# Kernel optimization log

Hardware: AMD Instinct MI355X
Metric: run time of the kernel (lower is better)

Reference implementation:

```python
import jax, jax.numpy as jnp
import numpy as np

D = 6          # atom_dims
K_AA = 17      # atom-atom knn (self dropped -> 16)
K_PE = 16      # point-atom knn
NEG = 0.2      # LeakyReLU slope
EPS = 1e-5     # GroupNorm eps
N_PTS, N_AT = 20000, 8000
H = 2 * D + 1  # MLP hidden width = 13


def lrelu(x):
    return jnp.where(x >= 0, x, NEG * x)


def linear(x, w, b):  # torch Linear convention: w is (out, in)
    return jnp.einsum('...i,oi->...o', x, w) + b


def group_norm(x, gamma, beta, groups):
    n, c = x.shape
    xg = x.reshape(n, groups, c // groups)
    mu = xg.mean(-1, keepdims=True)
    var = ((xg - mu) ** 2).mean(-1, keepdims=True)
    xn = ((xg - mu) * jax.lax.rsqrt(var + EPS)).reshape(n, c)
    return xn * gamma + beta


def knn(x, y, k):
    # squared euclidean distances via gram trick (memory-bound argKmin)
    d2 = jnp.sum(x * x, -1)[:, None] + jnp.sum(y * y, -1)[None, :] - 2.0 * (x @ y.T)
    _, idx = jax.lax.top_k(-jax.lax.stop_gradient(d2), k)
    # recompute dists from gathered coords (matches knn_atoms; differentiable)
    dists = jnp.sum((x[:, None, :] - y[idx]) ** 2, -1)  # (N, k)
    return idx, dists


def mp_block(self_feat, nb_source, idx, dists, w1, b1, w2, b2, gamma, beta, groups):
    n, k = idx.shape
    nb = nb_source[idx]  # (N, k, D) gather
    feat = jnp.concatenate([
        jnp.broadcast_to(self_feat[:, None, :], (n, k, self_feat.shape[1])),
        nb,
        dists[..., None],
    ], axis=-1)  # (N, k, 2D+1)
    msg = linear(lrelu(linear(feat, w1, b1)), w2, b2).sum(1)  # (N, D)
    return self_feat + lrelu(group_norm(msg, gamma, beta, groups))


def setup_inputs() -> dict:
    key = jax.random.key(0)
    ks = jax.random.split(key, 20)
    f = lambda k, s, sc=1.0: jax.random.normal(k, s, jnp.float32) * sc
    inp = {
        'xyz': f(ks[0], (N_PTS, 3), 10.0),
        'atom_xyz': f(ks[1], (N_AT, 3), 10.0),
        'atomtypes': f(ks[2], (N_AT, D)),
        'batch': jnp.zeros((N_PTS,), jnp.int32),
        'atom_batch': jnp.zeros((N_AT,), jnp.int32),
        # transform_types: Linear(D,D) -> LeakyReLU -> Linear(D,D)
        'tt_w1': f(ks[3], (D, D), 0.3), 'tt_b1': f(ks[4], (D,), 0.1),
        'tt_w2': f(ks[5], (D, D), 0.3), 'tt_b2': f(ks[6], (D,), 0.1),
        # atom_atom: 3 layers of Linear(13,13)->LeakyReLU->Linear(13,6), GroupNorm(2,6)
        'aa_w1': f(ks[7], (3, H, H), 0.3), 'aa_b1': f(ks[8], (3, H), 0.1),
        'aa_w2': f(ks[9], (3, D, H), 0.3), 'aa_b2': f(ks[10], (3, D), 0.1),
        'aa_gamma': jnp.ones((3, D), jnp.float32), 'aa_beta': jnp.zeros((3, D), jnp.float32),
        # embed: same shapes
        'em_w1': f(ks[11], (3, H, H), 0.3), 'em_b1': f(ks[12], (3, H), 0.1),
        'em_w2': f(ks[13], (3, D, H), 0.3), 'em_b2': f(ks[14], (3, D), 0.1),
        'em_gamma': jnp.ones((3, D), jnp.float32), 'em_beta': jnp.zeros((3, D), jnp.float32),
    }
    return inp


def reference(xyz, atom_xyz, atomtypes, batch, atom_batch,
              tt_w1, tt_b1, tt_w2, tt_b2,
              aa_w1, aa_b1, aa_w2, aa_b2, aa_gamma, aa_beta,
              em_w1, em_b1, em_w2, em_b2, em_gamma, em_beta):
    # batch / atom_batch are all-zero (single block), so full knn == ranged knn
    at = linear(lrelu(linear(atomtypes, tt_w1, tt_b1)), tt_w2, tt_b2)
    # Atom_Atom_embedding_MP: knn over atoms, drop self (first) neighbor
    idx, dists = knn(atom_xyz, atom_xyz, K_AA)
    idx, dists = idx[:, 1:], dists[:, 1:]
    out = at
    for i in range(3):
        out = mp_block(out, out, idx, dists,
                       aa_w1[i], aa_b1[i], aa_w2[i], aa_b2[i],
                       aa_gamma[i], aa_beta[i], 2)
    # Atom_embedding_MP: points gather from (fixed) atom features
    idx2, dists2 = knn(xyz, atom_xyz, K_PE)
    emb = jnp.ones((xyz.shape[0], D), xyz.dtype)
    for i in range(3):
        emb = mp_block(emb, out, idx2, dists2,
                       em_w1[i], em_b1[i], em_w2[i], em_b2[i],
                       em_gamma[i], em_beta[i], 2)
    return emb
```

## Files before the change

kernel.cpp:

```cpp
#include <hip/hip_runtime.h>
#include <cfloat>
#include <climits>

#define NEG 0.2f
#define GEPS 1e-5f
#define D 6
#define H 13
#define KOUT 16

#define MPAD 8192
#define TILE 1024
#define NTILES 8
#define P1TILES 4
#define QW 8
#define QBLK 32
#define CAP 64
#define KMAX 17
#define MARGIN 0.05f

__device__ __forceinline__ float lrelu(float x){ return x >= 0.f ? x : NEG*x; }

__global__ void prep_kernel(const float* __restrict__ atom_xyz,
                            const float* __restrict__ xyz,
                            const float* __restrict__ at_in,
                            const float* __restrict__ w1, const float* __restrict__ b1,
                            const float* __restrict__ w2, const float* __restrict__ b2,
                            float4* __restrict__ candP, float4* __restrict__ ptsP,
                            float* __restrict__ fa, int n_at, int n_pts){
  int i = blockIdx.x*blockDim.x + threadIdx.x;
  if (i < MPAD){
    if (i < n_at){
      float x = atom_xyz[3*i], y = atom_xyz[3*i+1], z = atom_xyz[3*i+2];
      float sq;
      {
#pragma clang fp contract(off)
        sq = (x*x + y*y) + z*z;
      }
      candP[i] = make_float4(x,y,z,sq);
    } else {
      candP[i] = make_float4(0.f,0.f,0.f,1e30f);
    }
  }
  if (i < n_pts){
    float x = xyz[3*i], y = xyz[3*i+1], z = xyz[3*i+2];
    float sq;
    {
#pragma clang fp contract(off)
      sq = (x*x + y*y) + z*z;
    }
    ptsP[i] = make_float4(x,y,z,sq);
  }
  if (i < n_at){
    float x[D], h[D];
    #pragma unroll
    for (int j=0;j<D;j++) x[j] = at_in[i*D+j];
    #pragma unroll
    for (int o=0;o<D;o++){
      float acc = b1[o];
      #pragma unroll
      for (int j=0;j<D;j++) acc += w1[o*D+j]*x[j];
      h[o] = lrelu(acc);
    }
    #pragma unroll
    for (int o=0;o<D;o++){
      float acc = b2[o];
      #pragma unroll
      for (int j=0;j<D;j++) acc += w2[o*D+j]*h[j];
      fa[i*D+o] = acc;
    }
  }
}

__device__ __forceinline__ void sort64fq(float (&v)[QW], int lane){
  #pragma unroll
  for (int k = 2; k <= 64; k <<= 1){
    #pragma unroll
    for (int j = k >> 1; j >= 1; j >>= 1){
      bool dir = ((lane & j) == 0) == ((lane & k) == 0);
      #pragma unroll
      for (int q = 0; q < QW; ++q){
        float o = __shfl_xor(v[q], j);
        v[q] = dir ? fminf(v[q], o) : fmaxf(v[q], o);
      }
    }
  }
}

__device__ __forceinline__ void sort64f1(float& a, int lane){
  #pragma unroll
  for (int k=2;k<=64;k<<=1){
    #pragma unroll
    for (int j=k>>1;j>=1;j>>=1){
      float o = __shfl_xor(a, j);
      bool dir = ((lane&j)==0)==((lane&k)==0);
      a = dir ? fminf(a,o) : fmaxf(a,o);
    }
  }
}

__device__ __forceinline__ void sort64pair(float& d, int& i, int lane){
  #pragma unroll
  for (int k = 2; k <= 64; k <<= 1){
    #pragma unroll
    for (int j = k >> 1; j >= 1; j >>= 1){
      float od = __shfl_xor(d, j);
      int   oi = __shfl_xor(i, j);
      bool lower = (lane & j) == 0;
      bool asc   = (lane & k) == 0;
      bool oless = (od < d) || (od == d && oi < i);
      bool take  = (lower == asc) ? oless : !oless;
      d = take ? od : d;
      i = take ? oi : i;
    }
  }
}

__global__ __launch_bounds__(256)
void knn10_kernel(const float4* __restrict__ candP, int ncand,
                  const float4* __restrict__ qarrA, int nqA, int nbA,
                  const float4* __restrict__ qarrB, int nqB,
                  int* __restrict__ oidxA, float* __restrict__ odistA,
                  int* __restrict__ oidxB, float* __restrict__ odistB){
  __shared__ float4 tile[TILE];
  __shared__ float4 qs[QBLK];
  __shared__ ushort slots[4][QW][CAP];
  __shared__ int    scnt[4][QW];

  const int tid  = threadIdx.x;
  const int w    = tid >> 6;
  const int lane = tid & 63;

  const bool taskA = (int)blockIdx.x < nbA;
  const int  bq    = taskA ? blockIdx.x : (blockIdx.x - nbA);
  const float4* __restrict__ qarr = taskA ? qarrA : qarrB;
  const int  nq    = taskA ? nqA : nqB;
  const int  ksel  = taskA ? 17 : 16;
  const int  ooff  = taskA ? 1  : 0;
  int*   __restrict__ oidx  = taskA ? oidxA  : oidxB;
  float* __restrict__ odist = taskA ? odistA : odistB;

  if (tid < QBLK){
    int qg = bq*QBLK + tid;
    qs[tid] = qarr[qg < nq ? qg : nq-1];
  }
  if (lane < QW) scnt[w][lane] = 0;
  __syncthreads();

  float q2x[QW], q2y[QW], q2z[QW];
  #pragma unroll
  for (int q = 0; q < QW; ++q){
    float4 v = qs[w*QW + q];
    q2x[q] = -2.f*v.x; q2y[q] = -2.f*v.y; q2z[q] = -2.f*v.z;
  }

  float mn[QW];
  #pragma unroll
  for (int q = 0; q < QW; ++q) mn[q] = FLT_MAX;

  for (int t = 0; t < P1TILES; ++t){
    #pragma unroll
    for (int u = 0; u < TILE/256; ++u)
      tile[tid + 256*u] = candP[t*TILE + tid + 256*u];
    __syncthreads();
    #pragma unroll 2
    for (int i = 0; i < TILE/64; ++i){
      float4 cv = tile[i*64 + lane];
      #pragma unroll
      for (int q = 0; q < QW; ++q){
        float e = fmaf(q2x[q], cv.x, fmaf(q2y[q], cv.y, fmaf(q2z[q], cv.z, cv.w)));
        mn[q] = fminf(mn[q], e);
      }
    }
    __syncthreads();
  }

  sort64fq(mn, lane);
  float T[QW];
  #pragma unroll
  for (int q = 0; q < QW; ++q) T[q] = __shfl(mn[q], ksel-1) + MARGIN;

  for (int t = 0; t < NTILES; ++t){
    #pragma unroll
    for (int u = 0; u < TILE/256; ++u)
      tile[tid + 256*u] = candP[t*TILE + tid + 256*u];
    __syncthreads();
    #pragma unroll 2
    for (int i = 0; i < TILE/64; ++i){
      float4 cv = tile[i*64 + lane];
      const int j = t*TILE + i*64 + lane;
      #pragma unroll
      for (int q = 0; q < QW; ++q){
        float e = fmaf(q2x[q], cv.x, fmaf(q2y[q], cv.y, fmaf(q2z[q], cv.z, cv.w)));
        if (e <= T[q]){
          int ofs = atomicAdd(&scnt[w][q], 1);
          if (ofs < CAP) slots[w][q][ofs] = (ushort)j;
        }
      }
    }
    __syncthreads();
  }

  for (int q = 0; q < QW; ++q){
    const int qgq = bq*QBLK + w*QW + q;
    if (qgq >= nq) continue;
    const float4 qv = qs[w*QW + q];
    int C = scnt[w][q];

    if (C > CAP){
      const float fq2x = -2.f*qv.x, fq2y = -2.f*qv.y, fq2z = -2.f*qv.z;
      float m = FLT_MAX;
      for (int j = lane; j < MPAD; j += 64){
        float4 cp = candP[j];
        float e = fmaf(fq2x, cp.x, fmaf(fq2y, cp.y, fmaf(fq2z, cp.z, cp.w)));
        m = fminf(m, e);
      }
      sort64f1(m, lane);
      const float T2 = __shfl(m, ksel-1) + MARGIN;
      int cnt = 0;
      const unsigned long long ltm = (1ULL << lane) - 1ULL;
      for (int j = lane; j < MPAD; j += 64){
        float4 cp = candP[j];
        float e = fmaf(fq2x, cp.x, fmaf(fq2y, cp.y, fmaf(fq2z, cp.z, cp.w)));
        bool acc = e <= T2;
        unsigned long long msk = __ballot(acc);
        if (acc){
          int ofs = cnt + __popcll(msk & ltm);
          if (ofs < CAP) slots[w][q][ofs] = (ushort)j;
        }
        cnt += __popcll(msk);
      }
      __threadfence_block();
      C = cnt;
    }

    if (C <= CAP){
      int g = INT_MAX; float d2 = FLT_MAX;
      if (lane < C){
        g = slots[w][q][lane];
        float4 cp = candP[g];
        {
#pragma clang fp contract(off)
          float dot = qv.x*cp.x + qv.y*cp.y + qv.z*cp.z;
          d2 = (qv.w + cp.w) - 2.0f*dot;
        }
      }
      sort64pair(d2, g, lane);
      if (lane >= ooff && lane < ooff + KOUT){
        float4 cp = candP[g];
        float dist;
        {
#pragma clang fp contract(off)
          float dx = qv.x-cp.x, dy = qv.y-cp.y, dz = qv.z-cp.z;
          dist = (dx*dx + dy*dy) + dz*dz;
        }
        oidx[(size_t)qgq*KOUT + (lane-ooff)]  = g;
        odist[(size_t)qgq*KOUT + (lane-ooff)] = dist;
      }
    } else if (lane == 0){
      float bd[KMAX]; int bi[KMAX];
      for (int t=0;t<ksel;t++){ bd[t]=FLT_MAX; bi[t]=INT_MAX; }
      float cmd = FLT_MAX; int cmi = INT_MAX;
      for (int jj = 0; jj < ncand; ++jj){
        float4 cp = candP[jj];
        float d2;
        {
#pragma clang fp contract(off)
          float dot = qv.x*cp.x + qv.y*cp.y + qv.z*cp.z;
          d2 = (qv.w + cp.w) - 2.0f*dot;
        }
        if (d2 < cmd || (d2 == cmd && jj < cmi)){
          int rt = 0; float rmd=-FLT_MAX; int rmi=-1;
          for (int t=0;t<ksel;t++){
            if (bd[t] > rmd || (bd[t]==rmd && bi[t]>rmi)){ rmd=bd[t]; rmi=bi[t]; rt=t; }
          }
          bd[rt]=d2; bi[rt]=jj;
          cmd=-FLT_MAX; cmi=-1;
          for (int t=0;t<ksel;t++){
            if (bd[t] > cmd || (bd[t]==cmd && bi[t]>cmi)){ cmd=bd[t]; cmi=bi[t]; }
          }
        }
      }
      for (int t=0;t<ksel;t++){
        int rt=-1; float mnd=FLT_MAX; int mni=INT_MAX;
        for (int u2=0;u2<ksel;u2++){
          if (bd[u2] < mnd || (bd[u2]==mnd && bi[u2]<mni)){ mnd=bd[u2]; mni=bi[u2]; rt=u2; }
        }
        bd[rt]=FLT_MAX; bi[rt]=INT_MAX;
        if (t >= ooff){
          float4 cp = candP[mni];
          float dist;
          {
#pragma clang fp contract(off)
            float dx=qv.x-cp.x, dy=qv.y-cp.y, dz=qv.z-cp.z;
            dist = (dx*dx + dy*dy) + dz*dz;
          }
          oidx[(size_t)qgq*KOUT + (t-ooff)]  = mni;
          odist[(size_t)qgq*KOUT + (t-ooff)] = dist;
        }
      }
    }
  }
}

template<bool SELF_ONES>
__global__ __launch_bounds__(256)
void mp_kernel(const float* __restrict__ self_feat,
               const float* __restrict__ nb_src,
               const int* __restrict__ idx,
               const float* __restrict__ dists,
               const float* __restrict__ w1g, const float* __restrict__ b1g,
               const float* __restrict__ w2g, const float* __restrict__ b2g,
               const float* __restrict__ gam, const float* __restrict__ bet,
               float* __restrict__ out, int n){
  __shared__ float w1[H*H], b1v[H], w2[D*H], b2v[D], gm[D], bt[D];
  for (int t=threadIdx.x; t<H*H; t+=blockDim.x) w1[t]=w1g[t];
  if (threadIdx.x < H) b1v[threadIdx.x]=b1g[threadIdx.x];
  for (int t=threadIdx.x; t<D*H; t+=blockDim.x) w2[t]=w2g[t];
  if (threadIdx.x < D){
    b2v[threadIdx.x]=b2g[threadIdx.x];
    gm[threadIdx.x]=gam[threadIdx.x];
    bt[threadIdx.x]=bet[threadIdx.x];
  }
  __syncthreads();
  int tt = blockIdx.x*blockDim.x + threadIdx.x;
  int p = tt >> 2, sub = tt & 3;
  if (p >= n) return;

  float s[D];
  #pragma unroll
  for (int j=0;j<D;j++) s[j] = SELF_ONES ? 1.0f : self_feat[p*D+j];
  float msg[D] = {0,0,0,0,0,0};

  #pragma unroll
  for (int u=0;u<KOUT/4;u++){
    int k = u*4 + sub;
    int j = idx[p*KOUT+k];
    float dd = dists[p*KOUT+k];
    float f[H];
    #pragma unroll
    for (int c=0;c<D;c++) f[c]=s[c];
    #pragma unroll
    for (int c=0;c<D;c++) f[D+c]=nb_src[j*D+c];
    f[2*D]=dd;
    float h[H];
    #pragma unroll
    for (int o=0;o<H;o++){
      float acc=b1v[o];
      #pragma unroll
      for (int c=0;c<H;c++) acc += w1[o*H+c]*f[c];
      h[o]=lrelu(acc);
    }
    #pragma unroll
    for (int o=0;o<D;o++){
      float acc=b2v[o];
      #pragma unroll
      for (int c=0;c<H;c++) acc += w2[o*H+c]*h[c];
      msg[o]+=acc;
    }
  }

  #pragma unroll
  for (int c=0;c<D;c++){
    msg[c] += __shfl_xor(msg[c], 1);
    msg[c] += __shfl_xor(msg[c], 2);
  }

  if (sub == 0){
    float y[D];
    #pragma unroll
    for (int gi=0; gi<2; gi++){
      float m0=msg[gi*3+0], m1=msg[gi*3+1], m2=msg[gi*3+2];
      float mu = ((m0+m1)+m2) / 3.0f;
      float d0=m0-mu, d1=m1-mu, d2v=m2-mu;
      float var = ((d0*d0 + d1*d1) + d2v*d2v) / 3.0f;
      float inv = 1.0f / sqrtf(var + GEPS);
      y[gi*3+0] = d0*inv;
      y[gi*3+1] = d1*inv;
      y[gi*3+2] = d2v*inv;
    }
    #pragma unroll
    for (int c=0;c<D;c++){
      float vv = y[c]*gm[c] + bt[c];
      out[p*D+c] = s[c] + lrelu(vv);
    }
  }
}

extern "C" void kernel_launch(void* const* d_in, const int* in_sizes, int n_in,
                              void* d_out, int out_size, void* d_ws, size_t ws_size,
                              hipStream_t stream){
  const float* xyz       = (const float*)d_in[0];
  const float* atom_xyz  = (const float*)d_in[1];
  const float* atomtypes = (const float*)d_in[2];
  const float* tt_w1 = (const float*)d_in[5];
  const float* tt_b1 = (const float*)d_in[6];
  const float* tt_w2 = (const float*)d_in[7];
  const float* tt_b2 = (const float*)d_in[8];
  const float* aa_w1 = (const float*)d_in[9];
  const float* aa_b1 = (const float*)d_in[10];
  const float* aa_w2 = (const float*)d_in[11];
  const float* aa_b2 = (const float*)d_in[12];
  const float* aa_gamma = (const float*)d_in[13];
  const float* aa_beta  = (const float*)d_in[14];
  const float* em_w1 = (const float*)d_in[15];
  const float* em_b1 = (const float*)d_in[16];
  const float* em_w2 = (const float*)d_in[17];
  const float* em_b2 = (const float*)d_in[18];
  const float* em_gamma = (const float*)d_in[19];
  const float* em_beta  = (const float*)d_in[20];

  const int n_pts = in_sizes[0]/3;
  const int n_at  = in_sizes[1]/3;

  char* ws = (char*)d_ws;
  float4* candP = (float4*)ws; ws += (size_t)MPAD*sizeof(float4);
  float4* ptsP  = (float4*)ws; ws += (size_t)n_pts*sizeof(float4);
  float* fa   = (float*)ws; ws += (size_t)n_at*D*4;
  float* fb   = (float*)ws; ws += (size_t)n_at*D*4;
  int*   idxA = (int*)ws;   ws += (size_t)n_at*KOUT*4;
  float* distA= (float*)ws; ws += (size_t)n_at*KOUT*4;
  int*   idxP = (int*)ws;   ws += (size_t)n_pts*KOUT*4;
  float* distP= (float*)ws; ws += (size_t)n_pts*KOUT*4;
  float* ea   = (float*)ws; ws += (size_t)n_pts*D*4;
  float* eb   = (float*)ws; ws += (size_t)n_pts*D*4;
  float* outf = (float*)d_out;

  const int nprep = (MPAD > n_pts ? MPAD : n_pts);
  prep_kernel<<<(nprep+255)/256,256,0,stream>>>(
      atom_xyz, xyz, atomtypes, tt_w1, tt_b1, tt_w2, tt_b2,
      candP, ptsP, fa, n_at, n_pts);

  const int nbA = (n_at  + QBLK - 1) / QBLK;
  const int nbB = (n_pts + QBLK - 1) / QBLK;
  knn10_kernel<<<nbA + nbB,256,0,stream>>>(
      candP, n_at, candP, n_at, nbA, ptsP, n_pts,
      idxA, distA, idxP, distP);

  mp_kernel<false><<<(n_at*4+255)/256,256,0,stream>>>(fa, fa, idxA, distA,
      aa_w1+0*H*H, aa_b1+0*H, aa_w2+0*D*H, aa_b2+0*D, aa_gamma+0*D, aa_beta+0*D, fb, n_at);
  mp_kernel<false><<<(n_at*4+255)/256,256,0,stream>>>(fb, fb, idxA, distA,
      aa_w1+1*H*H, aa_b1+1*H, aa_w2+1*D*H, aa_b2+1*D, aa_gamma+1*D, aa_beta+1*D, fa, n_at);
  mp_kernel<false><<<(n_at*4+255)/256,256,0,stream>>>(fa, fa, idxA, distA,
      aa_w1+2*H*H, aa_b1+2*H, aa_w2+2*D*H, aa_b2+2*D, aa_gamma+2*D, aa_beta+2*D, fb, n_at);

  mp_kernel<true ><<<(n_pts*4+255)/256,256,0,stream>>>(nullptr, fb, idxP, distP,
      em_w1+0*H*H, em_b1+0*H, em_w2+0*D*H, em_b2+0*D, em_gamma+0*D, em_beta+0*D, ea, n_pts);
  mp_kernel<false><<<(n_pts*4+255)/256,256,0,stream>>>(ea, fb, idxP, distP,
      em_w1+1*H*H, em_b1+1*H, em_w2+1*D*H, em_b2+1*D, em_gamma+1*D, em_beta+1*D, eb, n_pts);
  mp_kernel<false><<<(n_pts*4+255)/256,256,0,stream>>>(eb, fb, idxP, distP,
      em_w1+2*H*H, em_b1+2*H, em_w2+2*D*H, em_b2+2*D, em_gamma+2*D, em_beta+2*D, outf, n_pts);
}
```

Before: 179.3 us.

## Double-buffer candidate tiles, scan all tiles in pass one, drop overflow fallback

The KNN kernel now double-buffers candidate tiles in shared memory and prefetches the next tile into registers while the current one is processed. This removes one barrier per tile and overlaps global loads with compute. The first pass that estimates the threshold now scans all 8 tiles instead of 4, so the threshold is exact and the margin keeps candidate counts small. The fallback that rescanned all candidates when a query overflowed CAP slots is removed, so overflowing queries now fall through to whatever C>CAP handling remains, with a correctness risk if the overflow occurs.

```diff
diff --git a/kernel.cpp b/kernel.cpp
--- a/kernel.cpp
+++ b/kernel.cpp
@@ -11,7 +11,6 @@
 #define MPAD 8192
 #define TILE 1024
 #define NTILES 8
-#define P1TILES 4
 #define QW 8
 #define QBLK 32
 #define CAP 64
@@ -86,18 +85,6 @@
   }
 }
 
-__device__ __forceinline__ void sort64f1(float& a, int lane){
-  #pragma unroll
-  for (int k=2;k<=64;k<<=1){
-    #pragma unroll
-    for (int j=k>>1;j>=1;j>>=1){
-      float o = __shfl_xor(a, j);
-      bool dir = ((lane&j)==0)==((lane&k)==0);
-      a = dir ? fminf(a,o) : fmaxf(a,o);
-    }
-  }
-}
-
 __device__ __forceinline__ void sort64pair(float& d, int& i, int lane){
   #pragma unroll
   for (int k = 2; k <= 64; k <<= 1){
@@ -116,12 +103,12 @@
 }
 
 __global__ __launch_bounds__(256)
-void knn10_kernel(const float4* __restrict__ candP, int ncand,
+void knn11_kernel(const float4* __restrict__ candP, int ncand,
                   const float4* __restrict__ qarrA, int nqA, int nbA,
                   const float4* __restrict__ qarrB, int nqB,
                   int* __restrict__ oidxA, float* __restrict__ odistA,
                   int* __restrict__ oidxB, float* __restrict__ odistB){
-  __shared__ float4 tile[TILE];
+  __shared__ float4 tile[2][TILE];
   __shared__ float4 qs[QBLK];
   __shared__ ushort slots[4][QW][CAP];
   __shared__ int    scnt[4][QW];
@@ -144,6 +131,12 @@
     qs[tid] = qarr[qg < nq ? qg : nq-1];
   }
   if (lane < QW) scnt[w][lane] = 0;
+
+  float4 st[4];
+  #pragma unroll
+  for (int u = 0; u < 4; ++u) st[u] = candP[tid + 256*u];
+  #pragma unroll
+  for (int u = 0; u < 4; ++u) tile[0][tid + 256*u] = st[u];
   __syncthreads();
 
   float q2x[QW], q2y[QW], q2z[QW];
@@ -157,20 +150,25 @@
   #pragma unroll
   for (int q = 0; q < QW; ++q) mn[q] = FLT_MAX;
 
-  for (int t = 0; t < P1TILES; ++t){
-    #pragma unroll
-    for (int u = 0; u < TILE/256; ++u)
-      tile[tid + 256*u] = candP[t*TILE + tid + 256*u];
-    __syncthreads();
+  for (int t = 0; t < NTILES; ++t){
+    const int cur = t & 1;
+    if (t+1 < NTILES){
+      #pragma unroll
+      for (int u = 0; u < 4; ++u) st[u] = candP[(t+1)*TILE + tid + 256*u];
+    }
     #pragma unroll 2
     for (int i = 0; i < TILE/64; ++i){
-      float4 cv = tile[i*64 + lane];
+      float4 cv = tile[cur][i*64 + lane];
       #pragma unroll
       for (int q = 0; q < QW; ++q){
         float e = fmaf(q2x[q], cv.x, fmaf(q2y[q], cv.y, fmaf(q2z[q], cv.z, cv.w)));
         mn[q] = fminf(mn[q], e);
       }
     }
+    if (t+1 < NTILES){
+      #pragma unroll
+      for (int u = 0; u < 4; ++u) tile[cur^1][tid + 256*u] = st[u];
+    }
     __syncthreads();
   }
 
@@ -179,14 +177,21 @@
   #pragma unroll
   for (int q = 0; q < QW; ++q) T[q] = __shfl(mn[q], ksel-1) + MARGIN;
 
+  #pragma unroll
+  for (int u = 0; u < 4; ++u) st[u] = candP[tid + 256*u];
+  #pragma unroll
+  for (int u = 0; u < 4; ++u) tile[0][tid + 256*u] = st[u];
+  __syncthreads();
+
   for (int t = 0; t < NTILES; ++t){
-    #pragma unroll
-    for (int u = 0; u < TILE/256; ++u)
-      tile[tid + 256*u] = candP[t*TILE + tid + 256*u];
-    __syncthreads();
+    const int cur = t & 1;
+    if (t+1 < NTILES){
+      #pragma unroll
+      for (int u = 0; u < 4; ++u) st[u] = candP[(t+1)*TILE + tid + 256*u];
+    }
     #pragma unroll 2
     for (int i = 0; i < TILE/64; ++i){
-      float4 cv = tile[i*64 + lane];
+      float4 cv = tile[cur][i*64 + lane];
       const int j = t*TILE + i*64 + lane;
       #pragma unroll
       for (int q = 0; q < QW; ++q){
@@ -197,6 +202,10 @@
         }
       }
     }
+    if (t+1 < NTILES){
+      #pragma unroll
+      for (int u = 0; u < 4; ++u) tile[cur^1][tid + 256*u] = st[u];
+    }
     __syncthreads();
   }
 
@@ -204,34 +213,7 @@
     const int qgq = bq*QBLK + w*QW + q;
     if (qgq >= nq) continue;
     const float4 qv = qs[w*QW + q];
-    int C = scnt[w][q];
-
-    if (C > CAP){
-      const float fq2x = -2.f*qv.x, fq2y = -2.f*qv.y, fq2z = -2.f*qv.z;
-      float m = FLT_MAX;
-      for (int j = lane; j < MPAD; j += 64){
-        float4 cp = candP[j];
-        float e = fmaf(fq2x, cp.x, fmaf(fq2y, cp.y, fmaf(fq2z, cp.z, cp.w)));
-        m = fminf(m, e);
-      }
-      sort64f1(m, lane);
-      const float T2 = __shfl(m, ksel-1) + MARGIN;
-      int cnt = 0;
-      const unsigned long long ltm = (1ULL << lane) - 1ULL;
-      for (int j = lane; j < MPAD; j += 64){
-        float4 cp = candP[j];
-        float e = fmaf(fq2x, cp.x, fmaf(fq2y, cp.y, fmaf(fq2z, cp.z, cp.w)));
-        bool acc = e <= T2;
-        unsigned long long msk = __ballot(acc);
-        if (acc){
-          int ofs = cnt + __popcll(msk & ltm);
-          if (ofs < CAP) slots[w][q][ofs] = (ushort)j;
-        }
-        cnt += __popcll(msk);
-      }
-      __threadfence_block();
-      C = cnt;
-    }
+    const int C = scnt[w][q];
 
     if (C <= CAP){
       int g = INT_MAX; float d2 = FLT_MAX;
@@ -432,7 +414,7 @@
 
   const int nbA = (n_at  + QBLK - 1) / QBLK;
   const int nbB = (n_pts + QBLK - 1) / QBLK;
-  knn10_kernel<<<nbA + nbB,256,0,stream>>>(
+  knn11_kernel<<<nbA + nbB,256,0,stream>>>(
       candP, n_at, candP, n_at, nbA, ptsP, n_pts,
       idxA, distA, idxP, distP);
 
```

Result: no change. 176.5 us (-1.6%).
